# Optimization experiments

Hardware: AMD Instinct MI355X
Metric: run time of the kernel (lower is better)

The kernel has to match this reference:

```python
import jax, jax.numpy as jnp
import numpy as np
import math

B, T, C = 4, 2048, 1024
NH, D = 16, 64  # n_head, head_dim; NH * D == C


def setup_inputs() -> dict:
    key = jax.random.key(0)
    ks = jax.random.split(key, 7)
    std = 0.02
    return {
        "x": jax.random.normal(ks[0], (B, T, C), dtype=jnp.float32),
        "W_attn": jax.random.normal(ks[1], (C, 3 * C), dtype=jnp.float32) * std,
        "b_attn": jax.random.normal(ks[2], (3 * C,), dtype=jnp.float32) * std,
        "bQ": jax.random.normal(ks[3], (NH, D), dtype=jnp.float32) * 0.1 + 0.5,
        "bK": jax.random.normal(ks[4], (NH, D), dtype=jnp.float32) * 0.1 + 0.3,
        "W_proj": jax.random.normal(ks[5], (C, C), dtype=jnp.float32) * std,
        "b_proj": jax.random.normal(ks[6], (C,), dtype=jnp.float32) * std,
    }


def reference(x, W_attn, b_attn, bQ, bK, W_proj, b_proj):
    Bx, Tx, Cx = x.shape
    qkv = x @ W_attn + b_attn                      # [B, T, 3C]
    q, k, v = jnp.split(qkv, 3, axis=2)
    # [B, T, C] -> [B, NH, T, D]
    q = q.reshape(Bx, Tx, NH, D).transpose(0, 2, 1, 3)
    k = k.reshape(Bx, Tx, NH, D).transpose(0, 2, 1, 3)
    v = v.reshape(Bx, Tx, NH, D).transpose(0, 2, 1, 3)
    # per-head disorder bias added to Q and K before the dot product
    q = q + bQ[None, :, None, :]
    k = k + bK[None, :, None, :]
    scores = jnp.einsum('bhqd,bhkd->bhqk', q, k) / math.sqrt(D)  # [B, NH, T, T]
    causal = jnp.tril(jnp.ones((Tx, Tx), dtype=bool))
    scores = jnp.where(causal[None, None], scores, jnp.float32(-jnp.inf))
    att = jax.nn.softmax(scores, axis=-1)
    y = jnp.einsum('bhqk,bhkd->bhqd', att, v)      # [B, NH, T, D]
    y = y.transpose(0, 2, 1, 3).reshape(Bx, Tx, Cx)
    return y @ W_proj + b_proj
```

## Files before the change

kernel.cpp:

```cpp
#include <hip/hip_runtime.h>

typedef unsigned short u16;
typedef unsigned int u32;
typedef unsigned long long u64;
typedef __bf16 bf16x8 __attribute__((ext_vector_type(8)));
typedef float f32x4 __attribute__((ext_vector_type(4)));

#define B_  4
#define T_  2048
#define C_  1024
#define NH_ 16
#define D_  64
#define M_  (B_*T_)
#define N_QKV (3*C_)

#define ATTN_BLOCKS 1024

#define BARRIER()  __asm__ __volatile__("s_barrier" ::: "memory")
#define WAIT_VM4() __asm__ __volatile__("s_waitcnt vmcnt(4)" ::: "memory")
#define WAIT_VM8() __asm__ __volatile__("s_waitcnt vmcnt(8)" ::: "memory")
#define WAIT_VM0() __asm__ __volatile__("s_waitcnt vmcnt(0)" ::: "memory")
#define LGKM0()    __asm__ __volatile__("s_waitcnt lgkmcnt(0)" ::: "memory")

__device__ __forceinline__ void async_copy16(void* lds, const void* gptr) {
  __builtin_amdgcn_global_load_lds(
      (const __attribute__((address_space(1))) u32*)gptr,
      (__attribute__((address_space(3))) u32*)(u32)(uintptr_t)lds,
      16, 0, 0);
}

__device__ __forceinline__ u16 f2bf(float f) {
  union { float f; unsigned u; } c; c.f = f;
  unsigned u = c.u;
  unsigned r = (u + 0x7fffu + ((u >> 16) & 1u)) >> 16;
  return (u16)r;
}

__global__ __launch_bounds__(256) void conv_bf16(const float* __restrict__ in,
                                                 u16* __restrict__ out, int n) {
  int i = (blockIdx.x * 256 + threadIdx.x) * 4;
  if (i < n) {
    float4 f = *reinterpret_cast<const float4*>(in + i);
    u16 o[4] = { f2bf(f.x), f2bf(f.y), f2bf(f.z), f2bf(f.w) };
    *reinterpret_cast<uint2*>(out + i) = *reinterpret_cast<uint2*>(o);
  }
}

__global__ __launch_bounds__(256) void transpose_bf16(const float* __restrict__ in,
                                                      u16* __restrict__ out,
                                                      int K, int N) {
  __shared__ float tile[32][33];
  int bi = blockIdx.y;
  int bj = blockIdx.x;
  int tx = threadIdx.x & 31;
  int ty = threadIdx.x >> 5;
#pragma unroll
  for (int i = 0; i < 4; ++i) {
    int row = ty + i * 8;
    tile[row][tx] = in[(bi * 32 + row) * N + bj * 32 + tx];
  }
  __syncthreads();
#pragma unroll
  for (int i = 0; i < 4; ++i) {
    int row = ty + i * 8;
    out[(bj * 32 + row) * K + bi * 32 + tx] = f2bf(tile[tx][row]);
  }
}

__global__ __launch_bounds__(256, 2) void gemm_qkv(const u16* __restrict__ A,
                                                   const u16* __restrict__ Bt,
                                                   const float* __restrict__ b_attn,
                                                   const float* __restrict__ bQ,
                                                   const float* __restrict__ bK,
                                                   u16* __restrict__ qo,
                                                   u16* __restrict__ ko,
                                                   u16* __restrict__ vo) {
  const int K = C_;
  int bid = blockIdx.x;
  int wg = (bid & 7) * 192 + (bid >> 3);
  int bm = wg / 24, bn = wg % 24;

  int tid = threadIdx.x;
  int wid = tid >> 6, lane = tid & 63;
  int lm = lane & 15, lq = lane >> 4;
  int wm = (wid >> 1) * 64, wn = (wid & 1) * 64;

  __shared__ u16 As[2][128 * 64];
  __shared__ u16 Bs[2][128 * 64];

  f32x4 acc[4][4];
#pragma unroll
  for (int i = 0; i < 4; ++i)
#pragma unroll
    for (int j = 0; j < 4; ++j) acc[i][j] = (f32x4){0.f, 0.f, 0.f, 0.f};

  const u16* Ab = A + (size_t)(bm * 128) * K;
  const u16* Bb = Bt + (size_t)(bn * 128) * K;
  int srow = lane >> 3;
  int sgc  = ((lane & 7) ^ srow) * 8;

  auto stage = [&](int bb, int t) {
#pragma unroll
    for (int i = 0; i < 4; ++i) {
      int c = i * 4 + wid;
      async_copy16(&As[bb][c * 512], Ab + (size_t)(c * 8 + srow) * K + t * 64 + sgc);
      async_copy16(&Bs[bb][c * 512], Bb + (size_t)(c * 8 + srow) * K + t * 64 + sgc);
    }
  };

  stage(0, 0);
  const int NT = K / 64;
  for (int t = 0; t < NT; ++t) {
    int bb = t & 1;
    int tn = (t + 1 < NT) ? t + 1 : t;
    stage(bb ^ 1, tn);
    WAIT_VM8();
    BARRIER();
    bf16x8 af[4][2], bf[4][2];
#pragma unroll
    for (int mt = 0; mt < 4; ++mt) {
      const u16* base = &As[bb][(wm + mt * 16 + lm) * 64];
#pragma unroll
      for (int kh = 0; kh < 2; ++kh)
        af[mt][kh] = *reinterpret_cast<const bf16x8*>(base + (((kh * 4 + lq) ^ (lm & 7)) * 8));
    }
#pragma unroll
    for (int nt = 0; nt < 4; ++nt) {
      const u16* base = &Bs[bb][(wn + nt * 16 + lm) * 64];
#pragma unroll
      for (int kh = 0; kh < 2; ++kh)
        bf[nt][kh] = *reinterpret_cast<const bf16x8*>(base + (((kh * 4 + lq) ^ (lm & 7)) * 8));
    }
#pragma unroll
    for (int mt = 0; mt < 4; ++mt)
#pragma unroll
      for (int nt = 0; nt < 4; ++nt)
#pragma unroll
        for (int kh = 0; kh < 2; ++kh)
          acc[mt][nt] = __builtin_amdgcn_mfma_f32_16x16x32_bf16(af[mt][kh], bf[nt][kh],
                                                                acc[mt][nt], 0, 0, 0);
    LGKM0();
    BARRIER();
  }
  WAIT_VM0();

  const float qscale = 0.18033688011112042f;
#pragma unroll
  for (int mt = 0; mt < 4; ++mt) {
#pragma unroll
    for (int nt = 0; nt < 4; ++nt) {
#pragma unroll
      for (int r = 0; r < 4; ++r) {
        int m = bm * 128 + wm + mt * 16 + lq * 4 + r;
        int n = bn * 128 + wn + nt * 16 + lm;
        float val = acc[mt][nt][r] + b_attn[n];
        int sel = n >> 10;
        int c = n & 1023;
        int h = c >> 6;
        int d = c & 63;
        int b = m >> 11;
        int t = m & 2047;
        if (sel == 0)      qo[(((size_t)(b * NH_ + h) * T_) + t) * D_ + d] = f2bf((val + bQ[c]) * qscale);
        else if (sel == 1) ko[(((size_t)(b * NH_ + h) * T_) + t) * D_ + d] = f2bf(val + bK[c]);
        else               vo[(((size_t)(b * NH_ + h) * D_) + d) * T_ + t] = f2bf(val);
      }
    }
  }
}

__global__ __launch_bounds__(256, 4) void attn_kernel(const u16* __restrict__ q,
                                                      const u16* __restrict__ k,
                                                      const u16* __restrict__ vt,
                                                      u16* __restrict__ y) {
  int tid = threadIdx.x;
  int w = tid >> 6, lane = tid & 63;
  int lm = lane & 15, lq = lane >> 4;

  __shared__ u16 Ks[2][64 * 64];
  __shared__ u16 Vs[2][64 * 64];

  int srow = lane >> 3;
  int sg   = (lane & 7) ^ srow;

  int idx = blockIdx.x;
  int c8 = idx & 255, jq = idx >> 8;
  int a = c8 & 7, gq = c8 >> 3;
  int qt, bh;
  if (jq == 0)      { qt = 15 - a; bh = gq; }
  else if (jq == 1) { qt = 8 + a;  bh = 32 + gq; }
  else if (jq == 2) { qt = 7 - a;  bh = gq; }
  else              { qt = a;      bh = 32 + gq; }

  int b = bh >> 4, h = bh & 15;
  const int klast = 2 * qt + 1;
  const int qrow0 = qt * 128 + w * 32;

  const u16* qb = q + ((size_t)bh * T_ + qrow0) * D_;
  const u16* kb = k + (size_t)bh * T_ * D_;
  const u16* vb = vt + (size_t)bh * D_ * T_;

  auto stage_K = [&](int buf, int kbi) {
    const u16* gb = kb + (size_t)(kbi * 64) * 64;
#pragma unroll
    for (int j = 0; j < 2; ++j) {
      int c = w * 2 + j;
      async_copy16(&Ks[buf][c * 512], gb + (c * 8 + srow) * 64 + sg * 8);
    }
  };
  auto stage_V = [&](int buf, int kbi) {
    const u16* gb = vb + kbi * 64;
#pragma unroll
    for (int j = 0; j < 2; ++j) {
      int c = w * 2 + j;
      async_copy16(&Vs[buf][c * 512], gb + (size_t)(c * 8 + srow) * T_ + sg * 8);
    }
  };

  bf16x8 bq[2][2];
#pragma unroll
  for (int qt2 = 0; qt2 < 2; ++qt2) {
    const u16* qp = qb + (qt2 * 16 + lm) * D_ + lq * 8;
    bq[qt2][0] = *reinterpret_cast<const bf16x8*>(qp);
    bq[qt2][1] = *reinterpret_cast<const bf16x8*>(qp + 32);
  }

  const __bf16 one_ = (__bf16)1.0f;
  const bf16x8 ones = (bf16x8){one_, one_, one_, one_, one_, one_, one_, one_};

  f32x4 o[4][2], o5[2];
#pragma unroll
  for (int dt = 0; dt < 4; ++dt)
#pragma unroll
    for (int qt2 = 0; qt2 < 2; ++qt2) o[dt][qt2] = (f32x4){0.f, 0.f, 0.f, 0.f};
  o5[0] = (f32x4){0.f, 0.f, 0.f, 0.f};
  o5[1] = (f32x4){0.f, 0.f, 0.f, 0.f};
  float mprev[2] = {-1e30f, -1e30f};

  stage_K(0, 0); stage_V(0, 0);
  stage_K(1, 1); stage_V(1, 1);

  for (int kbi = 0; kbi <= klast; ++kbi) {
    int buf = kbi & 1;
    WAIT_VM4();
    BARRIER();

    bf16x8 kf[4][2];
#pragma unroll
    for (int kt = 0; kt < 4; ++kt) {
      const u16* base = &Ks[buf][(kt * 16 + lm) * 64];
      kf[kt][0] = *reinterpret_cast<const bf16x8*>(base + ((lq ^ (lm & 7)) * 8));
      kf[kt][1] = *reinterpret_cast<const bf16x8*>(base + (((4 + lq) ^ (lm & 7)) * 8));
    }

    f32x4 s[4][2];
    __builtin_amdgcn_s_setprio(1);
#pragma unroll
    for (int kt = 0; kt < 4; ++kt)
#pragma unroll
      for (int qt2 = 0; qt2 < 2; ++qt2) {
        f32x4 z = (f32x4){0.f, 0.f, 0.f, 0.f};
        z = __builtin_amdgcn_mfma_f32_16x16x32_bf16(kf[kt][0], bq[qt2][0], z, 0, 0, 0);
        z = __builtin_amdgcn_mfma_f32_16x16x32_bf16(kf[kt][1], bq[qt2][1], z, 0, 0, 0);
        s[kt][qt2] = z;
      }
    __builtin_amdgcn_s_setprio(0);

    bool maskt = (kbi * 64 + 63 > qrow0);
    bf16x8 pb[2][2];
#pragma unroll
    for (int qt2 = 0; qt2 < 2; ++qt2) {
      int qg = qrow0 + qt2 * 16 + lm;
      if (maskt) {
#pragma unroll
        for (int kt = 0; kt < 4; ++kt)
#pragma unroll
          for (int r = 0; r < 4; ++r) {
            int key = kbi * 64 + kt * 16 + lq * 4 + r;
            if (key > qg) s[kt][qt2][r] = -1e30f;
          }
      }
      float mx[4];
#pragma unroll
      for (int kt = 0; kt < 4; ++kt)
        mx[kt] = fmaxf(fmaxf(s[kt][qt2][0], s[kt][qt2][1]),
                       fmaxf(s[kt][qt2][2], s[kt][qt2][3]));
      float mval = fmaxf(fmaxf(mx[0], mx[1]), fmaxf(mx[2], mx[3]));
      mval = fmaxf(mval, __shfl_xor(mval, 16));
      mval = fmaxf(mval, __shfl_xor(mval, 32));
      float mold = mprev[qt2];
      if (__ballot(mval > mold + 8.f)) {
        float mnew = fmaxf(mold, mval);
        float alpha = __builtin_exp2f(mold - mnew);
#pragma unroll
        for (int dt = 0; dt < 4; ++dt) o[dt][qt2] *= alpha;
        o5[qt2] *= alpha;
        mprev[qt2] = mnew;
      }
      float m = mprev[qt2];
      unsigned pw[8];
#pragma unroll
      for (int kt = 0; kt < 4; ++kt) {
        unsigned pu[4];
#pragma unroll
        for (int r = 0; r < 4; ++r) {
          float p = __builtin_exp2f(s[kt][qt2][r] - m);
          union { float f; unsigned u; } cc; cc.f = p;
          pu[r] = cc.u;
        }
        pw[kt * 2]     = __builtin_amdgcn_perm(pu[1], pu[0], 0x07060302u);
        pw[kt * 2 + 1] = __builtin_amdgcn_perm(pu[3], pu[2], 0x07060302u);
      }
      union { unsigned u[4]; bf16x8 v; } b0, b1;
#pragma unroll
      for (int t = 0; t < 4; ++t) { b0.u[t] = pw[t]; b1.u[t] = pw[4 + t]; }
      pb[qt2][0] = b0.v;
      pb[qt2][1] = b1.v;
    }

    {
      int r7 = lm & 7;
      int h4 = (lq & 1) * 4;
      int g0 = lq >> 1;
#pragma unroll
      for (int dt = 0; dt < 4; ++dt) {
        const u16* vbase = &Vs[buf][(dt * 16 + lm) * 64];
        union { u64 qd[2]; bf16x8 v; } t0, t1;
        t0.qd[0] = *reinterpret_cast<const u64*>(vbase + ((g0 ^ r7) * 8) + h4);
        t0.qd[1] = *reinterpret_cast<const u64*>(vbase + (((g0 + 2) ^ r7) * 8) + h4);
        t1.qd[0] = *reinterpret_cast<const u64*>(vbase + (((g0 + 4) ^ r7) * 8) + h4);
        t1.qd[1] = *reinterpret_cast<const u64*>(vbase + (((g0 + 6) ^ r7) * 8) + h4);
        __builtin_amdgcn_s_setprio(1);
#pragma unroll
        for (int qt2 = 0; qt2 < 2; ++qt2) {
          o[dt][qt2] = __builtin_amdgcn_mfma_f32_16x16x32_bf16(t0.v, pb[qt2][0], o[dt][qt2], 0, 0, 0);
          o[dt][qt2] = __builtin_amdgcn_mfma_f32_16x16x32_bf16(t1.v, pb[qt2][1], o[dt][qt2], 0, 0, 0);
        }
        __builtin_amdgcn_s_setprio(0);
      }
#pragma unroll
      for (int qt2 = 0; qt2 < 2; ++qt2) {
        o5[qt2] = __builtin_amdgcn_mfma_f32_16x16x32_bf16(ones, pb[qt2][0], o5[qt2], 0, 0, 0);
        o5[qt2] = __builtin_amdgcn_mfma_f32_16x16x32_bf16(ones, pb[qt2][1], o5[qt2], 0, 0, 0);
      }
    }

    BARRIER();
    int nk = (kbi + 2 <= klast) ? kbi + 2 : klast;
    stage_K(buf, nk); stage_V(buf, nk);
  }

  WAIT_VM0();

#pragma unroll
  for (int qt2 = 0; qt2 < 2; ++qt2) {
    float inv = 1.f / o5[qt2][0];
    int qg = qrow0 + qt2 * 16 + lm;
#pragma unroll
    for (int dt = 0; dt < 4; ++dt) {
      u16 wb[4];
#pragma unroll
      for (int r = 0; r < 4; ++r) wb[r] = f2bf(o[dt][qt2][r] * inv);
      int d = dt * 16 + lq * 4;
      *reinterpret_cast<uint2*>(&y[((size_t)(b * T_ + qg) * NH_ + h) * D_ + d]) =
          *reinterpret_cast<uint2*>(wb);
    }
  }
}

__global__ __launch_bounds__(256, 2) void gemm_proj(const u16* __restrict__ A,
                                                    const u16* __restrict__ Bt,
                                                    const float* __restrict__ b_proj,
                                                    float* __restrict__ out) {
  const int K = C_, N = C_;
  int bid = blockIdx.x;
  int wg = (bid & 7) * 64 + (bid >> 3);
  int bm = wg / 8, bn = wg % 8;

  int tid = threadIdx.x;
  int wid = tid >> 6, lane = tid & 63;
  int lm = lane & 15, lq = lane >> 4;
  int wm = (wid >> 1) * 64, wn = (wid & 1) * 64;

  __shared__ u16 As[2][128 * 64];
  __shared__ u16 Bs[2][128 * 64];

  f32x4 acc[4][4];
#pragma unroll
  for (int i = 0; i < 4; ++i)
#pragma unroll
    for (int j = 0; j < 4; ++j) acc[i][j] = (f32x4){0.f, 0.f, 0.f, 0.f};

  const u16* Ab = A + (size_t)(bm * 128) * K;
  const u16* Bb = Bt + (size_t)(bn * 128) * K;
  int srow = lane >> 3;
  int sgc  = ((lane & 7) ^ srow) * 8;

  auto stage = [&](int bb, int t) {
#pragma unroll
    for (int i = 0; i < 4; ++i) {
      int c = i * 4 + wid;
      async_copy16(&As[bb][c * 512], Ab + (size_t)(c * 8 + srow) * K + t * 64 + sgc);
      async_copy16(&Bs[bb][c * 512], Bb + (size_t)(c * 8 + srow) * K + t * 64 + sgc);
    }
  };

  stage(0, 0);
  const int NT = K / 64;
  for (int t = 0; t < NT; ++t) {
    int bb = t & 1;
    int tn = (t + 1 < NT) ? t + 1 : t;
    stage(bb ^ 1, tn);
    WAIT_VM8();
    BARRIER();
    bf16x8 af[4][2], bf[4][2];
#pragma unroll
    for (int mt = 0; mt < 4; ++mt) {
      const u16* base = &As[bb][(wm + mt * 16 + lm) * 64];
#pragma unroll
      for (int kh = 0; kh < 2; ++kh)
        af[mt][kh] = *reinterpret_cast<const bf16x8*>(base + (((kh * 4 + lq) ^ (lm & 7)) * 8));
    }
#pragma unroll
    for (int nt = 0; nt < 4; ++nt) {
      const u16* base = &Bs[bb][(wn + nt * 16 + lm) * 64];
#pragma unroll
      for (int kh = 0; kh < 2; ++kh)
        bf[nt][kh] = *reinterpret_cast<const bf16x8*>(base + (((kh * 4 + lq) ^ (lm & 7)) * 8));
    }
#pragma unroll
    for (int mt = 0; mt < 4; ++mt)
#pragma unroll
      for (int nt = 0; nt < 4; ++nt)
#pragma unroll
        for (int kh = 0; kh < 2; ++kh)
          acc[mt][nt] = __builtin_amdgcn_mfma_f32_16x16x32_bf16(af[mt][kh], bf[nt][kh],
                                                                acc[mt][nt], 0, 0, 0);
    LGKM0();
    BARRIER();
  }
  WAIT_VM0();

#pragma unroll
  for (int mt = 0; mt < 4; ++mt) {
#pragma unroll
    for (int nt = 0; nt < 4; ++nt) {
#pragma unroll
      for (int r = 0; r < 4; ++r) {
        int m = bm * 128 + wm + mt * 16 + lq * 4 + r;
        int n = bn * 128 + wn + nt * 16 + lm;
        out[(size_t)m * N + n] = acc[mt][nt][r] + b_proj[n];
      }
    }
  }
}

extern "C" void kernel_launch(void* const* d_in, const int* in_sizes, int n_in,
                              void* d_out, int out_size, void* d_ws, size_t ws_size,
                              hipStream_t stream) {
  const float* x      = (const float*)d_in[0];
  const float* W_attn = (const float*)d_in[1];
  const float* b_attn = (const float*)d_in[2];
  const float* bQ     = (const float*)d_in[3];
  const float* bK     = (const float*)d_in[4];
  const float* W_proj = (const float*)d_in[5];
  const float* b_proj = (const float*)d_in[6];
  float* out = (float*)d_out;

  char* ws = (char*)d_ws;
  u16* xb  = (u16*)(ws);
  u16* WaT = (u16*)(ws + 16777216);
  u16* WpT = (u16*)(ws + 23068672);
  u16* qw  = (u16*)(ws + 25165824);
  u16* kw  = (u16*)(ws + 41943040);
  u16* vw  = (u16*)(ws + 58720256);
  u16* yw  = (u16*)(ws + 75497472);

  conv_bf16<<<M_ * C_ / (4 * 256), 256, 0, stream>>>(x, xb, M_ * C_);
  {
    dim3 g(N_QKV / 32, C_ / 32);
    transpose_bf16<<<g, 256, 0, stream>>>(W_attn, WaT, C_, N_QKV);
  }
  {
    dim3 g(C_ / 32, C_ / 32);
    transpose_bf16<<<g, 256, 0, stream>>>(W_proj, WpT, C_, C_);
  }
  gemm_qkv<<<(M_ / 128) * (N_QKV / 128), 256, 0, stream>>>(xb, WaT, b_attn, bQ, bK, qw, kw, vw);
  attn_kernel<<<ATTN_BLOCKS, 256, 0, stream>>>(qw, kw, vw, yw);
  gemm_proj<<<(M_ / 128) * (C_ / 128), 256, 0, stream>>>(yw, WpT, b_proj, out);
}
```

Baseline: 325.7 us.

## Drop LDS staging in attention; load K/V directly from global per wave

Removes the double-buffered LDS staging of K and V tiles and the block barriers, so each wave reads K and V fragments straight from global memory (relying on L1/L2 caching). Each wave now stops at its own causal limit instead of the block-wide limit, and the block-to-tile mapping changes to a new ordering table. Work per wave also loses the s_setprio hints. This avoids barrier stalls and idle waves at the diagonal, but the four waves of a block now fetch the same K/V data redundantly and load latency is no longer hidden by async prefetch.

```diff
diff --git a/kernel.cpp b/kernel.cpp
--- a/kernel.cpp
+++ b/kernel.cpp
@@ -17,7 +17,6 @@
 #define ATTN_BLOCKS 1024
 
 #define BARRIER()  __asm__ __volatile__("s_barrier" ::: "memory")
-#define WAIT_VM4() __asm__ __volatile__("s_waitcnt vmcnt(4)" ::: "memory")
 #define WAIT_VM8() __asm__ __volatile__("s_waitcnt vmcnt(8)" ::: "memory")
 #define WAIT_VM0() __asm__ __volatile__("s_waitcnt vmcnt(0)" ::: "memory")
 #define LGKM0()    __asm__ __volatile__("s_waitcnt lgkmcnt(0)" ::: "memory")
@@ -176,45 +175,20 @@
   int w = tid >> 6, lane = tid & 63;
   int lm = lane & 15, lq = lane >> 4;
 
-  __shared__ u16 Ks[2][64 * 64];
-  __shared__ u16 Vs[2][64 * 64];
-
-  int srow = lane >> 3;
-  int sg   = (lane & 7) ^ srow;
-
-  int idx = blockIdx.x;
-  int c8 = idx & 255, jq = idx >> 8;
-  int a = c8 & 7, gq = c8 >> 3;
-  int qt, bh;
-  if (jq == 0)      { qt = 15 - a; bh = gq; }
-  else if (jq == 1) { qt = 8 + a;  bh = 32 + gq; }
-  else if (jq == 2) { qt = 7 - a;  bh = gq; }
-  else              { qt = a;      bh = 32 + gq; }
+  int bidx = blockIdx.x;
+  int x = bidx & 7;
+  int g = bidx >> 3;
+  const u64 ORD = 0x321074568BA9CDEFull;
+  int qt = (int)((ORD >> ((g >> 3) * 4)) & 15);
+  int bh = x + 8 * (g & 7);
 
   int b = bh >> 4, h = bh & 15;
-  const int klast = 2 * qt + 1;
   const int qrow0 = qt * 128 + w * 32;
+  const int klast = (qrow0 + 31) >> 6;
 
   const u16* qb = q + ((size_t)bh * T_ + qrow0) * D_;
   const u16* kb = k + (size_t)bh * T_ * D_;
   const u16* vb = vt + (size_t)bh * D_ * T_;
-
-  auto stage_K = [&](int buf, int kbi) {
-    const u16* gb = kb + (size_t)(kbi * 64) * 64;
-#pragma unroll
-    for (int j = 0; j < 2; ++j) {
-      int c = w * 2 + j;
-      async_copy16(&Ks[buf][c * 512], gb + (c * 8 + srow) * 64 + sg * 8);
-    }
-  };
-  auto stage_V = [&](int buf, int kbi) {
-    const u16* gb = vb + kbi * 64;
-#pragma unroll
-    for (int j = 0; j < 2; ++j) {
-      int c = w * 2 + j;
-      async_copy16(&Vs[buf][c * 512], gb + (size_t)(c * 8 + srow) * T_ + sg * 8);
-    }
-  };
 
   bf16x8 bq[2][2];
 #pragma unroll
@@ -236,24 +210,17 @@
   o5[1] = (f32x4){0.f, 0.f, 0.f, 0.f};
   float mprev[2] = {-1e30f, -1e30f};
 
-  stage_K(0, 0); stage_V(0, 0);
-  stage_K(1, 1); stage_V(1, 1);
-
   for (int kbi = 0; kbi <= klast; ++kbi) {
-    int buf = kbi & 1;
-    WAIT_VM4();
-    BARRIER();
-
+    const u16* ktb = kb + (size_t)(kbi * 64) * D_;
     bf16x8 kf[4][2];
 #pragma unroll
     for (int kt = 0; kt < 4; ++kt) {
-      const u16* base = &Ks[buf][(kt * 16 + lm) * 64];
-      kf[kt][0] = *reinterpret_cast<const bf16x8*>(base + ((lq ^ (lm & 7)) * 8));
-      kf[kt][1] = *reinterpret_cast<const bf16x8*>(base + (((4 + lq) ^ (lm & 7)) * 8));
+      const u16* kr = ktb + (kt * 16 + lm) * D_ + lq * 8;
+      kf[kt][0] = *reinterpret_cast<const bf16x8*>(kr);
+      kf[kt][1] = *reinterpret_cast<const bf16x8*>(kr + 32);
     }
 
     f32x4 s[4][2];
-    __builtin_amdgcn_s_setprio(1);
 #pragma unroll
     for (int kt = 0; kt < 4; ++kt)
 #pragma unroll
@@ -263,7 +230,6 @@
         z = __builtin_amdgcn_mfma_f32_16x16x32_bf16(kf[kt][1], bq[qt2][1], z, 0, 0, 0);
         s[kt][qt2] = z;
       }
-    __builtin_amdgcn_s_setprio(0);
 
     bool maskt = (kbi * 64 + 63 > qrow0);
     bf16x8 pb[2][2];
@@ -318,24 +284,20 @@
     }
 
     {
-      int r7 = lm & 7;
-      int h4 = (lq & 1) * 4;
-      int g0 = lq >> 1;
+      int t0 = kbi * 64;
 #pragma unroll
       for (int dt = 0; dt < 4; ++dt) {
-        const u16* vbase = &Vs[buf][(dt * 16 + lm) * 64];
-        union { u64 qd[2]; bf16x8 v; } t0, t1;
-        t0.qd[0] = *reinterpret_cast<const u64*>(vbase + ((g0 ^ r7) * 8) + h4);
-        t0.qd[1] = *reinterpret_cast<const u64*>(vbase + (((g0 + 2) ^ r7) * 8) + h4);
-        t1.qd[0] = *reinterpret_cast<const u64*>(vbase + (((g0 + 4) ^ r7) * 8) + h4);
-        t1.qd[1] = *reinterpret_cast<const u64*>(vbase + (((g0 + 6) ^ r7) * 8) + h4);
-        __builtin_amdgcn_s_setprio(1);
+        const u16* vr = vb + (size_t)(dt * 16 + lm) * T_ + t0;
+        union { u64 qd[2]; bf16x8 v; } a0, a1;
+        a0.qd[0] = *reinterpret_cast<const u64*>(vr + lq * 4);
+        a0.qd[1] = *reinterpret_cast<const u64*>(vr + 16 + lq * 4);
+        a1.qd[0] = *reinterpret_cast<const u64*>(vr + 32 + lq * 4);
+        a1.qd[1] = *reinterpret_cast<const u64*>(vr + 48 + lq * 4);
 #pragma unroll
         for (int qt2 = 0; qt2 < 2; ++qt2) {
-          o[dt][qt2] = __builtin_amdgcn_mfma_f32_16x16x32_bf16(t0.v, pb[qt2][0], o[dt][qt2], 0, 0, 0);
-          o[dt][qt2] = __builtin_amdgcn_mfma_f32_16x16x32_bf16(t1.v, pb[qt2][1], o[dt][qt2], 0, 0, 0);
+          o[dt][qt2] = __builtin_amdgcn_mfma_f32_16x16x32_bf16(a0.v, pb[qt2][0], o[dt][qt2], 0, 0, 0);
+          o[dt][qt2] = __builtin_amdgcn_mfma_f32_16x16x32_bf16(a1.v, pb[qt2][1], o[dt][qt2], 0, 0, 0);
         }
-        __builtin_amdgcn_s_setprio(0);
       }
 #pragma unroll
       for (int qt2 = 0; qt2 < 2; ++qt2) {
@@ -343,13 +305,7 @@
         o5[qt2] = __builtin_amdgcn_mfma_f32_16x16x32_bf16(ones, pb[qt2][1], o5[qt2], 0, 0, 0);
       }
     }
-
-    BARRIER();
-    int nk = (kbi + 2 <= klast) ? kbi + 2 : klast;
-    stage_K(buf, nk); stage_V(buf, nk);
-  }
-
-  WAIT_VM0();
+  }
 
 #pragma unroll
   for (int qt2 = 0; qt2 < 2; ++qt2) {
```

Measured after the change: 417.8 us. 1.28x slower.
